# Kernel optimization log

Measured on AMD Instinct MI355X. Metric: run time of the kernel, lower is better.

The kernel has to match this reference:

```python
import jax, jax.numpy as jnp
import numpy as np

N_LAYER = 4
N_EMBD = 768
N_HEAD = 12
B, T = 4, 1024  # T = 4 * t, t = 256 (block_size)
EPS = 1e-5


def layernorm(x, g, b):
    mu = jnp.mean(x, axis=-1, keepdims=True)
    var = jnp.var(x, axis=-1, keepdims=True)
    return (x - mu) * jax.lax.rsqrt(var + EPS) * g + b


def setup_inputs() -> dict:
    key = jax.random.key(0)
    ks = jax.random.split(key, 20)
    C, L, H = N_EMBD, N_LAYER, 4 * N_EMBD
    std = 0.02
    inp = {
        "x": jax.random.normal(ks[0], (B, T, C), dtype=jnp.float32),
        "ln1_g": jnp.ones((L, C), jnp.float32),
        "ln1_b": jnp.zeros((L, C), jnp.float32),
        "Wq": std * jax.random.normal(ks[1], (L, C, C), jnp.float32),
        "bq": jnp.zeros((L, C), jnp.float32),
        "Wk": std * jax.random.normal(ks[2], (L, C, C), jnp.float32),
        "bk": jnp.zeros((L, C), jnp.float32),
        "Wv": std * jax.random.normal(ks[3], (L, C, C), jnp.float32),
        "bv": jnp.zeros((L, C), jnp.float32),
        "Wp": std * jax.random.normal(ks[4], (L, C, C), jnp.float32),
        "bp": jnp.zeros((L, C), jnp.float32),
        "ln2_g": jnp.ones((L, C), jnp.float32),
        "ln2_b": jnp.zeros((L, C), jnp.float32),
        "W1": std * jax.random.normal(ks[5], (L, C, H), jnp.float32),
        "b1": jnp.zeros((L, H), jnp.float32),
        "W2": std * jax.random.normal(ks[6], (L, H, C), jnp.float32),
        "b2": jnp.zeros((L, C), jnp.float32),
    }
    return inp


def _forward(x, ln1_g, ln1_b, Wq, bq, Wk, bk, Wv, bv, Wp, bp, ln2_g, ln2_b, W1, b1, W2, b2):
    Bx, Tx, C = x.shape
    hd = C // N_HEAD
    t = Tx // 4
    # cross-conditional mask: causal tril(t,t) tiled 4x4 over the 4 streams
    mask = jnp.tile(jnp.tril(jnp.ones((t, t), dtype=bool)), (4, 4))  # [T, T]
    scale = 1.0 / np.sqrt(hd).astype(np.float32)

    def block(h, p):
        (g1, b1g, wq, bqv, wk, bkv, wv, bvv, wp, bpv, g2, b2g, w1, b1v, w2, b2v) = p
        a_in = layernorm(h, g1, b1g)
        q = (a_in @ wq + bqv).reshape(Bx, Tx, N_HEAD, hd).transpose(0, 2, 1, 3)
        k = (a_in @ wk + bkv).reshape(Bx, Tx, N_HEAD, hd).transpose(0, 2, 1, 3)
        v = (a_in @ wv + bvv).reshape(Bx, Tx, N_HEAD, hd).transpose(0, 2, 1, 3)
        att = jnp.einsum('bhqd,bhkd->bhqk', q, k) * scale
        att = jnp.where(mask, att, -jnp.inf)
        att = jax.nn.softmax(att, axis=-1)
        y = jnp.einsum('bhqk,bhkd->bhqd', att, v)
        y = y.transpose(0, 2, 1, 3).reshape(Bx, Tx, C)
        h = h + (y @ wp + bpv)
        m_in = layernorm(h, g2, b2g)
        m = jax.nn.gelu(m_in @ w1 + b1v, approximate=False) @ w2 + b2v
        return h + m, None

    params = (ln1_g, ln1_b, Wq, bq, Wk, bk, Wv, bv, Wp, bp, ln2_g, ln2_b, W1, b1, W2, b2)
    x, _ = jax.lax.scan(block, x, params)
    return x


def reference(x, ln1_g, ln1_b, Wq, bq, Wk, bk, Wv, bv, Wp, bp, ln2_g, ln2_b, W1, b1, W2, b2):
    return _forward(x, ln1_g, ln1_b, Wq, bq, Wk, bk, Wv, bv, Wp, bp, ln2_g, ln2_b, W1, b1, W2, b2)
```

## Files before the change

### kernel.cpp

```cpp
#include <hip/hip_runtime.h>
#include <hip/hip_bf16.h>
#include <math.h>

typedef __hip_bfloat16 bf16;
typedef __attribute__((ext_vector_type(8))) short bf16x8;
typedef __attribute__((ext_vector_type(4))) short s16x4;
typedef __attribute__((ext_vector_type(4))) float f32x4;

#define CDIM 768
#define HDIM 64
#define NHEAD 12
#define TSEQ 1024
#define MROWS 4096
#define HID 3072
#define QKVN 2304

__device__ inline void gld16(const void* g, void* l) {
  __builtin_amdgcn_global_load_lds((const __attribute__((address_space(1))) void*)g,
                                   (__attribute__((address_space(3))) void*)l, 16, 0, 0);
}
__device__ inline short f2bs(float f) { bf16 h = __float2bfloat16(f); return *reinterpret_cast<short*>(&h); }

__global__ void k_trans(const float* __restrict__ Wq, const float* __restrict__ Wk,
                        const float* __restrict__ Wv, const float* __restrict__ Wp,
                        const float* __restrict__ W1, const float* __restrict__ W2,
                        const float* __restrict__ bq, const float* __restrict__ bk,
                        const float* __restrict__ bv,
                        bf16* __restrict__ wqkv, bf16* __restrict__ wtp,
                        bf16* __restrict__ wt1, bf16* __restrict__ wt2,
                        float* __restrict__ bqkv) {
  __shared__ float t[32][33];
  int blk = blockIdx.x;
  int l = blk / 6921; blk -= l * 6921;
  Wq += (size_t)l * CDIM * CDIM; Wk += (size_t)l * CDIM * CDIM;
  Wv += (size_t)l * CDIM * CDIM; Wp += (size_t)l * CDIM * CDIM;
  W1 += (size_t)l * CDIM * HID;  W2 += (size_t)l * HID * CDIM;
  bq += (size_t)l * CDIM; bk += (size_t)l * CDIM; bv += (size_t)l * CDIM;
  wqkv += (size_t)l * QKVN * CDIM; wtp += (size_t)l * CDIM * CDIM;
  wt1  += (size_t)l * CDIM * HID;  wt2 += (size_t)l * CDIM * HID;
  bqkv += (size_t)l * QKVN;
  if (blk >= 6912) {
    int i = (blk - 6912) * 256 + threadIdx.y * 32 + threadIdx.x;
    if (i < QKVN) bqkv[i] = (i < CDIM) ? bq[i] : (i < 2 * CDIM) ? bk[i - CDIM] : bv[i - 2 * CDIM];
    return;
  }
  const float* src; bf16* dst; int K, N, n0, k0;
  if (blk < 1728) {
    int w = blk / 576, id = blk % 576;
    src = (w == 0) ? Wq : (w == 1) ? Wk : Wv;
    dst = wqkv + (size_t)w * CDIM * CDIM;
    K = CDIM; N = CDIM;
    n0 = (id % 24) * 32; k0 = (id / 24) * 32;
  } else if (blk < 2304) {
    int id = blk - 1728;
    src = Wp; dst = wtp; K = CDIM; N = CDIM;
    n0 = (id % 24) * 32; k0 = (id / 24) * 32;
  } else if (blk < 4608) {
    int id = blk - 2304;
    src = W1; dst = wt1; K = CDIM; N = HID;
    n0 = (id % 96) * 32; k0 = (id / 96) * 32;
  } else {
    int id = blk - 4608;
    src = W2; dst = wt2; K = HID; N = CDIM;
    n0 = (id % 24) * 32; k0 = (id / 24) * 32;
  }
  int c = threadIdx.x, ry = threadIdx.y;
  #pragma unroll
  for (int i = 0; i < 4; i++) {
    int r = ry + 8 * i;
    t[r][c] = src[(size_t)(k0 + r) * N + n0 + c];
  }
  __syncthreads();
  #pragma unroll
  for (int i = 0; i < 4; i++) {
    int r = ry + 8 * i;
    dst[(size_t)(n0 + r) * K + k0 + c] = __float2bfloat16(t[c][r]);
  }
}

__global__ __launch_bounds__(256) void k_ln(const float* __restrict__ h, const float* __restrict__ g,
                                            const float* __restrict__ b, bf16* __restrict__ out) {
  int wave = threadIdx.x >> 6, lane = threadIdx.x & 63;
  int row = blockIdx.x * 4 + wave;
  const float4* hr = (const float4*)(h + (size_t)row * CDIM);
  float4 v[3];
  float s = 0.f, ss = 0.f;
  #pragma unroll
  for (int i = 0; i < 3; i++) {
    v[i] = hr[lane * 3 + i];
    s  += v[i].x + v[i].y + v[i].z + v[i].w;
    ss += v[i].x * v[i].x + v[i].y * v[i].y + v[i].z * v[i].z + v[i].w * v[i].w;
  }
  #pragma unroll
  for (int off = 32; off > 0; off >>= 1) {
    s  += __shfl_xor(s, off, 64);
    ss += __shfl_xor(ss, off, 64);
  }
  float mu = s * (1.0f / CDIM);
  float var = ss * (1.0f / CDIM) - mu * mu;
  float rstd = rsqrtf(var + 1e-5f);
  const float4* gp = (const float4*)g;
  const float4* bp = (const float4*)b;
  s16x4* orow = (s16x4*)(out + (size_t)row * CDIM);
  #pragma unroll
  for (int i = 0; i < 3; i++) {
    float4 gg = gp[lane * 3 + i], bb = bp[lane * 3 + i];
    s16x4 o;
    o.x = f2bs((v[i].x - mu) * rstd * gg.x + bb.x);
    o.y = f2bs((v[i].y - mu) * rstd * gg.y + bb.y);
    o.z = f2bs((v[i].z - mu) * rstd * gg.z + bb.z);
    o.w = f2bs((v[i].w - mu) * rstd * gg.w + bb.w);
    orow[lane * 3 + i] = o;
  }
}


template <int BM, int BN, int EPI>
__global__ __launch_bounds__(256) void k_gemmT(const bf16* __restrict__ A, const bf16* __restrict__ Bt,
                                               const float* __restrict__ bias,
                                               void* __restrict__ outv, int M, int N, int K) {
  constexpr int MR = BM / 32, NR = BN / 32;
  __shared__ __align__(16) bf16 As[BM * 64];
  __shared__ __align__(16) bf16 Bs[BN * 64];
  int tid = threadIdx.x;
  int m0 = blockIdx.x * BM, n0 = blockIdx.y * BN;
  int wave = tid >> 6, lane = tid & 63;
  int wr = wave >> 1, wc = wave & 1;
  int lrow = lane & 15, quad = lane >> 4;
  int sw = lrow & 7;
  f32x4 zz = {0.f, 0.f, 0.f, 0.f};
  f32x4 acc[MR][NR];
  #pragma unroll
  for (int i = 0; i < MR; i++)
    #pragma unroll
    for (int j = 0; j < NR; j++) acc[i][j] = zz;
  const bf16* Ag = A + (size_t)m0 * K;
  const bf16* Bg = Bt + (size_t)n0 * K;
  for (int k0 = 0; k0 < K; k0 += 64) {
    __syncthreads();
    #pragma unroll
    for (int i = 0; i < BM / 32; i++) {
      int idx = i * 256 + tid;
      int row = idx >> 3, c = idx & 7;
      gld16(Ag + (size_t)row * K + k0 + ((c ^ (row & 7)) * 8), As + idx * 8);
    }
    #pragma unroll
    for (int i = 0; i < BN / 32; i++) {
      int idx = i * 256 + tid;
      int row = idx >> 3, c = idx & 7;
      gld16(Bg + (size_t)row * K + k0 + ((c ^ (row & 7)) * 8), Bs + idx * 8);
    }
    __syncthreads();
    #pragma unroll
    for (int kc = 0; kc < 2; kc++) {
      int g = kc * 4 + quad;
      bf16x8 af[MR], bfr[NR];
      #pragma unroll
      for (int mi = 0; mi < MR; mi++)
        af[mi] = *(const bf16x8*)(As + (wr * (BM / 2) + mi * 16 + lrow) * 64 + ((g ^ sw) * 8));
      #pragma unroll
      for (int ni = 0; ni < NR; ni++)
        bfr[ni] = *(const bf16x8*)(Bs + (wc * (BN / 2) + ni * 16 + lrow) * 64 + ((g ^ sw) * 8));
      #pragma unroll
      for (int mi = 0; mi < MR; mi++)
        #pragma unroll
        for (int ni = 0; ni < NR; ni++)
          acc[mi][ni] = __builtin_amdgcn_mfma_f32_16x16x32_bf16(af[mi], bfr[ni], acc[mi][ni], 0, 0, 0);
    }
  }
  #pragma unroll
  for (int ni = 0; ni < NR; ni++) {
    int gc = n0 + wc * (BN / 2) + ni * 16 + lrow;
    float bval = bias[gc];
    #pragma unroll
    for (int mi = 0; mi < MR; mi++) {
      #pragma unroll
      for (int r = 0; r < 4; r++) {
        int grow = m0 + wr * (BM / 2) + mi * 16 + quad * 4 + r;
        float vv = acc[mi][ni][r] + bval;
        if (EPI == 1) vv = 0.5f * vv * (1.0f + erff(vv * 0.70710678118654752f));
        if (EPI == 2) {
          float* hp = (float*)outv + (size_t)grow * N + gc;
          *hp = *hp + vv;
        } else {
          ((bf16*)outv)[(size_t)grow * N + gc] = __float2bfloat16(vv);
        }
      }
    }
  }
}

__global__ __launch_bounds__(256) void k_attn(const bf16* __restrict__ qkv, bf16* __restrict__ y) {
  int bh = blockIdx.x;
  int b = bh / NHEAD, hh = bh % NHEAD;
  int qc = blockIdx.y;
  int tid = threadIdx.x;
  int wave = tid >> 6, lane = tid & 63;
  int lrow = lane & 15, quad = lane >> 4;
  int sw = lrow & 7;
  int q0 = qc * 64 + wave * 16;
  int qmod = q0 & 255;
  int qcmod = (qc * 64) & 255;

  const size_t rstride = QKVN;
  const bf16* qbase = qkv + (size_t)(b * TSEQ) * rstride + hh * HDIM;
  const bf16* kbase = qbase + CDIM;
  const bf16* vbase = qbase + 2 * CDIM;

  bf16x8 qf[2];
  #pragma unroll
  for (int kc = 0; kc < 2; kc++)
    qf[kc] = *(const bf16x8*)(qbase + (size_t)(q0 + lrow) * rstride + kc * 32 + quad * 8);

  f32x4 zz = {0.f, 0.f, 0.f, 0.f};
  f32x4 Oacc[4];
  #pragma unroll
  for (int j = 0; j < 4; j++) Oacc[j] = zz;
  float m[4] = {-1e30f, -1e30f, -1e30f, -1e30f};
  float l[4] = {0.f, 0.f, 0.f, 0.f};

  __shared__ __align__(16) bf16 Ks[64 * 64];
  __shared__ __align__(16) bf16 Vt[64 * 72];
  __shared__ __align__(16) bf16 Pl[4][16 * 64];

  for (int kt = 0; kt < 16; kt++) {
    int k0 = kt * 64;
    int kmod = k0 & 255;
    if (kmod > qcmod + 63) continue;
    __syncthreads();
    #pragma unroll
    for (int i = 0; i < 2; i++) {
      int idx = i * 256 + tid;
      int key = idx >> 3, c = idx & 7;
      gld16(kbase + (size_t)(k0 + key) * rstride + ((c ^ (key & 7)) * 8), Ks + idx * 8);
      int vkey = idx & 63, vd0 = (idx >> 6) * 8;
      bf16x8 vv = *(const bf16x8*)(vbase + (size_t)(k0 + vkey) * rstride + vd0);
      const bf16* vp = (const bf16*)&vv;
      #pragma unroll
      for (int j = 0; j < 8; j++) Vt[(vd0 + j) * 72 + vkey] = vp[j];
    }
    __syncthreads();
    if (kmod > qmod + 15) continue;

    f32x4 s[4];
    #pragma unroll
    for (int sub = 0; sub < 4; sub++) {
      s[sub] = zz;
      #pragma unroll
      for (int kc = 0; kc < 2; kc++) {
        int g = kc * 4 + quad;
        bf16x8 kf = *(const bf16x8*)(Ks + (sub * 16 + lrow) * 64 + ((g ^ sw) * 8));
        s[sub] = __builtin_amdgcn_mfma_f32_16x16x32_bf16(qf[kc], kf, s[sub], 0, 0, 0);
      }
    }
    bool partial = (kmod + 63 > qmod);
    #pragma unroll
    for (int sub = 0; sub < 4; sub++)
      #pragma unroll
      for (int r = 0; r < 4; r++) {
        float sv = s[sub][r] * 0.125f;
        if (partial) {
          int krel = kmod + sub * 16 + lrow;
          int qrel = qmod + quad * 4 + r;
          if (krel > qrel) sv = -1e30f;
        }
        s[sub][r] = sv;
      }
    float pr[4][4], alpha[4];
    #pragma unroll
    for (int r = 0; r < 4; r++) {
      float v = fmaxf(fmaxf(s[0][r], s[1][r]), fmaxf(s[2][r], s[3][r]));
      v = fmaxf(v, __shfl_xor(v, 1, 64));
      v = fmaxf(v, __shfl_xor(v, 2, 64));
      v = fmaxf(v, __shfl_xor(v, 4, 64));
      v = fmaxf(v, __shfl_xor(v, 8, 64));
      float mnew = fmaxf(m[r], v);
      alpha[r] = __expf(m[r] - mnew);
      m[r] = mnew;
      float rsum = 0.f;
      #pragma unroll
      for (int sub = 0; sub < 4; sub++) {
        pr[sub][r] = __expf(s[sub][r] - mnew);
        rsum += pr[sub][r];
      }
      rsum += __shfl_xor(rsum, 1, 64);
      rsum += __shfl_xor(rsum, 2, 64);
      rsum += __shfl_xor(rsum, 4, 64);
      rsum += __shfl_xor(rsum, 8, 64);
      l[r] = l[r] * alpha[r] + rsum;
    }
    #pragma unroll
    for (int j = 0; j < 4; j++)
      #pragma unroll
      for (int r = 0; r < 4; r++) Oacc[j][r] *= alpha[r];
    bf16* Pw = (bf16*)Pl[wave];
    #pragma unroll
    for (int sub = 0; sub < 4; sub++) {
      int cc = sub * 2 + (lrow >> 3);
      int e = lrow & 7;
      #pragma unroll
      for (int r = 0; r < 4; r++) {
        int mm = quad * 4 + r;
        Pw[mm * 64 + ((cc ^ (mm & 7)) * 8) + e] = __float2bfloat16(pr[sub][r]);
      }
    }
    bf16x8 pf[2];
    #pragma unroll
    for (int kc = 0; kc < 2; kc++) {
      int g = kc * 4 + quad;
      pf[kc] = *(const bf16x8*)(Pw + lrow * 64 + ((g ^ sw) * 8));
    }
    #pragma unroll
    for (int j = 0; j < 4; j++)
      #pragma unroll
      for (int kc = 0; kc < 2; kc++) {
        bf16x8 vf = *(const bf16x8*)(Vt + (j * 16 + lrow) * 72 + kc * 32 + quad * 8);
        Oacc[j] = __builtin_amdgcn_mfma_f32_16x16x32_bf16(pf[kc], vf, Oacc[j], 0, 0, 0);
      }
  }
  #pragma unroll
  for (int r = 0; r < 4; r++) {
    float inv = 1.0f / l[r];
    bf16* yp = y + (size_t)(b * TSEQ + q0 + quad * 4 + r) * CDIM + hh * HDIM;
    #pragma unroll
    for (int j = 0; j < 4; j++)
      yp[j * 16 + lrow] = __float2bfloat16(Oacc[j][r] * inv);
  }
}

extern "C" void kernel_launch(void* const* d_in, const int* in_sizes, int n_in,
                              void* d_out, int out_size, void* d_ws, size_t ws_size,
                              hipStream_t stream) {
  const float* x    = (const float*)d_in[0];
  const float* ln1g = (const float*)d_in[1];
  const float* ln1b = (const float*)d_in[2];
  const float* Wq   = (const float*)d_in[3];
  const float* bq   = (const float*)d_in[4];
  const float* Wk   = (const float*)d_in[5];
  const float* bk   = (const float*)d_in[6];
  const float* Wv   = (const float*)d_in[7];
  const float* bv   = (const float*)d_in[8];
  const float* Wp   = (const float*)d_in[9];
  const float* bp   = (const float*)d_in[10];
  const float* ln2g = (const float*)d_in[11];
  const float* ln2b = (const float*)d_in[12];
  const float* W1   = (const float*)d_in[13];
  const float* b1   = (const float*)d_in[14];
  const float* W2   = (const float*)d_in[15];
  const float* b2   = (const float*)d_in[16];

  char* ws = (char*)d_ws;
  size_t off = 0;
  float* h    = (float*)(ws + off); off += (size_t)MROWS * CDIM * 4;
  bf16* a     = (bf16*)(ws + off);  off += (size_t)MROWS * CDIM * 2;
  bf16* qkvb  = (bf16*)(ws + off);  off += (size_t)MROWS * QKVN * 2;
  bf16* yb    = (bf16*)(ws + off);  off += (size_t)MROWS * CDIM * 2;
  bf16* m1    = qkvb;

  const size_t szQkv = (size_t)QKVN * CDIM * 2;
  const size_t szP   = (size_t)CDIM * CDIM * 2;
  const size_t szW1  = (size_t)CDIM * HID * 2;
  const size_t szW2  = (size_t)CDIM * HID * 2;
  const size_t szB   = (size_t)QKVN * 4;
  const size_t wlayer = szQkv + szP + szW1 + szW2 + szB;
  bool hoist = ws_size >= off + 4 * wlayer + 4096;
  int nW = hoist ? 4 : 1;

  bf16* wqkv  = (bf16*)(ws + off);  off += nW * szQkv;
  bf16* wtp   = (bf16*)(ws + off);  off += nW * szP;
  bf16* wt1   = (bf16*)(ws + off);  off += nW * szW1;
  bf16* wt2   = (bf16*)(ws + off);  off += nW * szW2;
  float* bqkv = (float*)(ws + off); off += nW * szB;

  int n = MROWS * CDIM;
  hipMemcpyAsync(h, x, (size_t)n * sizeof(float), hipMemcpyDeviceToDevice, stream);

  if (hoist)
    k_trans<<<dim3(4 * 6921), dim3(32, 8), 0, stream>>>(Wq, Wk, Wv, Wp, W1, W2, bq, bk, bv,
                                                        wqkv, wtp, wt1, wt2, bqkv);

  for (int l = 0; l < 4; l++) {
    int wl = hoist ? l : 0;
    if (!hoist)
      k_trans<<<dim3(6921), dim3(32, 8), 0, stream>>>(
          Wq + (size_t)l * CDIM * CDIM, Wk + (size_t)l * CDIM * CDIM,
          Wv + (size_t)l * CDIM * CDIM, Wp + (size_t)l * CDIM * CDIM,
          W1 + (size_t)l * CDIM * HID, W2 + (size_t)l * HID * CDIM,
          bq + (size_t)l * CDIM, bk + (size_t)l * CDIM, bv + (size_t)l * CDIM,
          wqkv, wtp, wt1, wt2, bqkv);
    const bf16* wqkvl = wqkv + (size_t)wl * QKVN * CDIM;
    const bf16* wtpl  = wtp  + (size_t)wl * CDIM * CDIM;
    const bf16* wt1l  = wt1  + (size_t)wl * CDIM * HID;
    const bf16* wt2l  = wt2  + (size_t)wl * CDIM * HID;
    const float* bqkvl = bqkv + (size_t)wl * QKVN;

    k_ln<<<dim3(MROWS / 4), dim3(256), 0, stream>>>(h, ln1g + l * CDIM, ln1b + l * CDIM, a);

    k_gemmT<64, 128, 0><<<dim3(MROWS / 64, QKVN / 128), dim3(256), 0, stream>>>(
        a, wqkvl, bqkvl, qkvb, MROWS, QKVN, CDIM);

    k_attn<<<dim3(4 * NHEAD, 16), dim3(256), 0, stream>>>(qkvb, yb);

    k_gemmT<64, 64, 2><<<dim3(MROWS / 64, CDIM / 64), dim3(256), 0, stream>>>(
        yb, wtpl, bp + (size_t)l * CDIM, h, MROWS, CDIM, CDIM);

    k_ln<<<dim3(MROWS / 4), dim3(256), 0, stream>>>(h, ln2g + l * CDIM, ln2b + l * CDIM, a);

    k_gemmT<64, 128, 1><<<dim3(MROWS / 64, HID / 128), dim3(256), 0, stream>>>(
        a, wt1l, b1 + (size_t)l * HID, m1, MROWS, HID, CDIM);

    k_gemmT<64, 64, 2><<<dim3(MROWS / 64, CDIM / 64), dim3(256), 0, stream>>>(
        m1, wt2l, b2 + (size_t)l * CDIM, h, MROWS, CDIM, HID);
  }

  hipMemcpyAsync(d_out, h, (size_t)n * sizeof(float), hipMemcpyDeviceToDevice, stream);
}
```

Before: 881.1 us.

## Write V transposed from QKV GEMM epilogue and restructure attention softmax layout

The QKV GEMM epilogue now writes the V columns into a per-head transposed buffer, so the attention kernel can async-load V tiles into swizzled LDS with global_load_lds. This replaces the per-element scalar transpose into LDS that the old code did on every key tile. The S MFMA operands are swapped so each lane holds one query row, which reduces the row max and sum to two cross-lane shuffles and allows vectorised stores of P. Query-chunk scheduling is also permuted. The cost is an extra V buffer and scattered 8-byte epilogue stores.

Result: faster. 776.4 us (-11.9%).

```diff
diff --git a/kernel.cpp b/kernel.cpp
--- a/kernel.cpp
+++ b/kernel.cpp
@@ -5,6 +5,7 @@
 typedef __hip_bfloat16 bf16;
 typedef __attribute__((ext_vector_type(8))) short bf16x8;
 typedef __attribute__((ext_vector_type(4))) short s16x4;
+typedef __attribute__((ext_vector_type(4))) unsigned short u16x4;
 typedef __attribute__((ext_vector_type(4))) float f32x4;
 
 #define CDIM 768
@@ -118,7 +119,8 @@
 template <int BM, int BN, int EPI>
 __global__ __launch_bounds__(256) void k_gemmT(const bf16* __restrict__ A, const bf16* __restrict__ Bt,
                                                const float* __restrict__ bias,
-                                               void* __restrict__ outv, int M, int N, int K) {
+                                               void* __restrict__ outv, bf16* __restrict__ out2,
+                                               int M, int N, int K) {
   constexpr int MR = BM / 32, NR = BN / 32;
   __shared__ __align__(16) bf16 As[BM * 64];
   __shared__ __align__(16) bf16 Bs[BN * 64];
@@ -174,26 +176,39 @@
     float bval = bias[gc];
     #pragma unroll
     for (int mi = 0; mi < MR; mi++) {
-      #pragma unroll
-      for (int r = 0; r < 4; r++) {
-        int grow = m0 + wr * (BM / 2) + mi * 16 + quad * 4 + r;
-        float vv = acc[mi][ni][r] + bval;
-        if (EPI == 1) vv = 0.5f * vv * (1.0f + erff(vv * 0.70710678118654752f));
-        if (EPI == 2) {
-          float* hp = (float*)outv + (size_t)grow * N + gc;
-          *hp = *hp + vv;
-        } else {
-          ((bf16*)outv)[(size_t)grow * N + gc] = __float2bfloat16(vv);
+      if (EPI == 3 && gc >= 1536) {
+        int dcol = gc - 1536, h2 = dcol >> 6, dd = dcol & 63;
+        int grow0 = m0 + wr * (BM / 2) + mi * 16 + quad * 4;
+        u16x4 o;
+        o.x = (unsigned short)f2bs(acc[mi][ni][0] + bval);
+        o.y = (unsigned short)f2bs(acc[mi][ni][1] + bval);
+        o.z = (unsigned short)f2bs(acc[mi][ni][2] + bval);
+        o.w = (unsigned short)f2bs(acc[mi][ni][3] + bval);
+        int bh2 = (grow0 >> 10) * NHEAD + h2;
+        *(u16x4*)(out2 + ((size_t)bh2 * HDIM + dd) * TSEQ + (grow0 & 1023)) = o;
+      } else {
+        #pragma unroll
+        for (int r = 0; r < 4; r++) {
+          int grow = m0 + wr * (BM / 2) + mi * 16 + quad * 4 + r;
+          float vv = acc[mi][ni][r] + bval;
+          if (EPI == 1) vv = 0.5f * vv * (1.0f + erff(vv * 0.70710678118654752f));
+          if (EPI == 2) {
+            float* hp = (float*)outv + (size_t)grow * N + gc;
+            *hp = *hp + vv;
+          } else {
+            ((bf16*)outv)[(size_t)grow * N + gc] = __float2bfloat16(vv);
+          }
         }
       }
     }
   }
 }
 
-__global__ __launch_bounds__(256) void k_attn(const bf16* __restrict__ qkv, bf16* __restrict__ y) {
+__global__ __launch_bounds__(256) void k_attn(const bf16* __restrict__ qkv, const bf16* __restrict__ vt,
+                                              bf16* __restrict__ y) {
   int bh = blockIdx.x;
   int b = bh / NHEAD, hh = bh % NHEAD;
-  int qc = blockIdx.y;
+  int qc = blockIdx.y ^ 3;
   int tid = threadIdx.x;
   int wave = tid >> 6, lane = tid & 63;
   int lrow = lane & 15, quad = lane >> 4;
@@ -205,7 +220,7 @@
   const size_t rstride = QKVN;
   const bf16* qbase = qkv + (size_t)(b * TSEQ) * rstride + hh * HDIM;
   const bf16* kbase = qbase + CDIM;
-  const bf16* vbase = qbase + 2 * CDIM;
+  const bf16* vtb = vt + (size_t)bh * HDIM * TSEQ;
 
   bf16x8 qf[2];
   #pragma unroll
@@ -216,11 +231,10 @@
   f32x4 Oacc[4];
   #pragma unroll
   for (int j = 0; j < 4; j++) Oacc[j] = zz;
-  float m[4] = {-1e30f, -1e30f, -1e30f, -1e30f};
-  float l[4] = {0.f, 0.f, 0.f, 0.f};
+  float m = -1e30f, l = 0.f;
 
   __shared__ __align__(16) bf16 Ks[64 * 64];
-  __shared__ __align__(16) bf16 Vt[64 * 72];
+  __shared__ __align__(16) bf16 Vs[64 * 64];
   __shared__ __align__(16) bf16 Pl[4][16 * 64];
 
   for (int kt = 0; kt < 16; kt++) {
@@ -231,13 +245,9 @@
     #pragma unroll
     for (int i = 0; i < 2; i++) {
       int idx = i * 256 + tid;
-      int key = idx >> 3, c = idx & 7;
-      gld16(kbase + (size_t)(k0 + key) * rstride + ((c ^ (key & 7)) * 8), Ks + idx * 8);
-      int vkey = idx & 63, vd0 = (idx >> 6) * 8;
-      bf16x8 vv = *(const bf16x8*)(vbase + (size_t)(k0 + vkey) * rstride + vd0);
-      const bf16* vp = (const bf16*)&vv;
-      #pragma unroll
-      for (int j = 0; j < 8; j++) Vt[(vd0 + j) * 72 + vkey] = vp[j];
+      int row = idx >> 3, c = idx & 7;
+      gld16(kbase + (size_t)(k0 + row) * rstride + ((c ^ (row & 7)) * 8), Ks + idx * 8);
+      gld16(vtb + (size_t)row * TSEQ + k0 + ((c ^ (row & 7)) * 8), Vs + idx * 8);
     }
     __syncthreads();
     if (kmod > qmod + 15) continue;
@@ -250,59 +260,56 @@
       for (int kc = 0; kc < 2; kc++) {
         int g = kc * 4 + quad;
         bf16x8 kf = *(const bf16x8*)(Ks + (sub * 16 + lrow) * 64 + ((g ^ sw) * 8));
-        s[sub] = __builtin_amdgcn_mfma_f32_16x16x32_bf16(qf[kc], kf, s[sub], 0, 0, 0);
+        s[sub] = __builtin_amdgcn_mfma_f32_16x16x32_bf16(kf, qf[kc], s[sub], 0, 0, 0);
       }
     }
     bool partial = (kmod + 63 > qmod);
+    int qrel = qmod + lrow;
     #pragma unroll
     for (int sub = 0; sub < 4; sub++)
       #pragma unroll
       for (int r = 0; r < 4; r++) {
         float sv = s[sub][r] * 0.125f;
-        if (partial) {
-          int krel = kmod + sub * 16 + lrow;
-          int qrel = qmod + quad * 4 + r;
-          if (krel > qrel) sv = -1e30f;
-        }
+        if (partial && (kmod + sub * 16 + quad * 4 + r > qrel)) sv = -1e30f;
         s[sub][r] = sv;
       }
-    float pr[4][4], alpha[4];
+    float mx = fmaxf(fmaxf(fmaxf(s[0][0], s[0][1]), fmaxf(s[0][2], s[0][3])),
+                     fmaxf(fmaxf(s[1][0], s[1][1]), fmaxf(s[1][2], s[1][3])));
+    mx = fmaxf(mx, fmaxf(fmaxf(fmaxf(s[2][0], s[2][1]), fmaxf(s[2][2], s[2][3])),
+                         fmaxf(fmaxf(s[3][0], s[3][1]), fmaxf(s[3][2], s[3][3]))));
+    mx = fmaxf(mx, __shfl_xor(mx, 16, 64));
+    mx = fmaxf(mx, __shfl_xor(mx, 32, 64));
+    float mnew = fmaxf(m, mx);
+    float alpha = __expf(m - mnew);
+    m = mnew;
+    float p[4][4];
+    float rs = 0.f;
+    #pragma unroll
+    for (int sub = 0; sub < 4; sub++)
+      #pragma unroll
+      for (int r = 0; r < 4; r++) {
+        p[sub][r] = __expf(s[sub][r] - mnew);
+        rs += p[sub][r];
+      }
+    rs += __shfl_xor(rs, 16, 64);
+    rs += __shfl_xor(rs, 32, 64);
+    l = l * alpha + rs;
     #pragma unroll
     for (int r = 0; r < 4; r++) {
-      float v = fmaxf(fmaxf(s[0][r], s[1][r]), fmaxf(s[2][r], s[3][r]));
-      v = fmaxf(v, __shfl_xor(v, 1, 64));
-      v = fmaxf(v, __shfl_xor(v, 2, 64));
-      v = fmaxf(v, __shfl_xor(v, 4, 64));
-      v = fmaxf(v, __shfl_xor(v, 8, 64));
-      float mnew = fmaxf(m[r], v);
-      alpha[r] = __expf(m[r] - mnew);
-      m[r] = mnew;
-      float rsum = 0.f;
-      #pragma unroll
-      for (int sub = 0; sub < 4; sub++) {
-        pr[sub][r] = __expf(s[sub][r] - mnew);
-        rsum += pr[sub][r];
-      }
-      rsum += __shfl_xor(rsum, 1, 64);
-      rsum += __shfl_xor(rsum, 2, 64);
-      rsum += __shfl_xor(rsum, 4, 64);
-      rsum += __shfl_xor(rsum, 8, 64);
-      l[r] = l[r] * alpha[r] + rsum;
-    }
-    #pragma unroll
-    for (int j = 0; j < 4; j++)
-      #pragma unroll
-      for (int r = 0; r < 4; r++) Oacc[j][r] *= alpha[r];
+      float ar = __shfl(alpha, quad * 4 + r, 16);
+      #pragma unroll
+      for (int j = 0; j < 4; j++) Oacc[j][r] *= ar;
+    }
     bf16* Pw = (bf16*)Pl[wave];
     #pragma unroll
     for (int sub = 0; sub < 4; sub++) {
-      int cc = sub * 2 + (lrow >> 3);
-      int e = lrow & 7;
-      #pragma unroll
-      for (int r = 0; r < 4; r++) {
-        int mm = quad * 4 + r;
-        Pw[mm * 64 + ((cc ^ (mm & 7)) * 8) + e] = __float2bfloat16(pr[sub][r]);
-      }
+      u16x4 o;
+      o.x = (unsigned short)f2bs(p[sub][0]);
+      o.y = (unsigned short)f2bs(p[sub][1]);
+      o.z = (unsigned short)f2bs(p[sub][2]);
+      o.w = (unsigned short)f2bs(p[sub][3]);
+      int ch = sub * 2 + (quad >> 1);
+      *(u16x4*)(Pw + lrow * 64 + ((ch ^ sw) * 8) + 4 * (quad & 1)) = o;
     }
     bf16x8 pf[2];
     #pragma unroll
@@ -314,17 +321,18 @@
     for (int j = 0; j < 4; j++)
       #pragma unroll
       for (int kc = 0; kc < 2; kc++) {
-        bf16x8 vf = *(const bf16x8*)(Vt + (j * 16 + lrow) * 72 + kc * 32 + quad * 8);
+        int g = kc * 4 + quad;
+        bf16x8 vf = *(const bf16x8*)(Vs + (j * 16 + lrow) * 64 + ((g ^ sw) * 8));
         Oacc[j] = __builtin_amdgcn_mfma_f32_16x16x32_bf16(pf[kc], vf, Oacc[j], 0, 0, 0);
       }
   }
   #pragma unroll
   for (int r = 0; r < 4; r++) {
-    float inv = 1.0f / l[r];
+    float linv = 1.0f / __shfl(l, quad * 4 + r, 16);
     bf16* yp = y + (size_t)(b * TSEQ + q0 + quad * 4 + r) * CDIM + hh * HDIM;
     #pragma unroll
     for (int j = 0; j < 4; j++)
-      yp[j * 16 + lrow] = __float2bfloat16(Oacc[j][r] * inv);
+      yp[j * 16 + lrow] = __float2bfloat16(Oacc[j][r] * linv);
   }
 }
 
@@ -355,6 +363,7 @@
   bf16* a     = (bf16*)(ws + off);  off += (size_t)MROWS * CDIM * 2;
   bf16* qkvb  = (bf16*)(ws + off);  off += (size_t)MROWS * QKVN * 2;
   bf16* yb    = (bf16*)(ws + off);  off += (size_t)MROWS * CDIM * 2;
+  bf16* vt    = (bf16*)(ws + off);  off += (size_t)4 * NHEAD * HDIM * TSEQ * 2;
   bf16* m1    = qkvb;
 
   const size_t szQkv = (size_t)QKVN * CDIM * 2;
@@ -396,21 +405,21 @@
 
     k_ln<<<dim3(MROWS / 4), dim3(256), 0, stream>>>(h, ln1g + l * CDIM, ln1b + l * CDIM, a);
 
-    k_gemmT<64, 128, 0><<<dim3(MROWS / 64, QKVN / 128), dim3(256), 0, stream>>>(
-        a, wqkvl, bqkvl, qkvb, MROWS, QKVN, CDIM);
-
-    k_attn<<<dim3(4 * NHEAD, 16), dim3(256), 0, stream>>>(qkvb, yb);
+    k_gemmT<64, 128, 3><<<dim3(MROWS / 64, QKVN / 128), dim3(256), 0, stream>>>(
+        a, wqkvl, bqkvl, qkvb, vt, MROWS, QKVN, CDIM);
+
+    k_attn<<<dim3(4 * NHEAD, 16), dim3(256), 0, stream>>>(qkvb, vt, yb);
 
     k_gemmT<64, 64, 2><<<dim3(MROWS / 64, CDIM / 64), dim3(256), 0, stream>>>(
-        yb, wtpl, bp + (size_t)l * CDIM, h, MROWS, CDIM, CDIM);
+        yb, wtpl, bp + (size_t)l * CDIM, h, nullptr, MROWS, CDIM, CDIM);
 
     k_ln<<<dim3(MROWS / 4), dim3(256), 0, stream>>>(h, ln2g + l * CDIM, ln2b + l * CDIM, a);
 
     k_gemmT<64, 128, 1><<<dim3(MROWS / 64, HID / 128), dim3(256), 0, stream>>>(
-        a, wt1l, b1 + (size_t)l * HID, m1, MROWS, HID, CDIM);
+        a, wt1l, b1 + (size_t)l * HID, m1, nullptr, MROWS, HID, CDIM);
 
     k_gemmT<64, 64, 2><<<dim3(MROWS / 64, CDIM / 64), dim3(256), 0, stream>>>(
-        m1, wt2l, b2 + (size_t)l * CDIM, h, MROWS, CDIM, HID);
+        m1, wt2l, b2 + (size_t)l * CDIM, h, nullptr, MROWS, CDIM, HID);
   }
 
   hipMemcpyAsync(d_out, h, (size_t)n * sizeof(float), hipMemcpyDeviceToDevice, stream);
```
